# Kernel optimization log

Hardware: AMD Instinct MI355X
Metric: run time of the kernel (lower is better)

Reference implementation:

```python
import jax, jax.numpy as jnp
import numpy as np

H = 1024       # hidden_size
NH = 16        # num heads
HD = H // NH   # head dim
EPS = 1e-12


def setup_inputs() -> dict:
    key = jax.random.key(0)
    ks = jax.random.split(key, 12)
    s = 1.0 / np.sqrt(H)
    return {
        "hidden_states": jax.random.normal(ks[0], (2, 2048, H), jnp.float32),
        "attention_mask": jnp.zeros((2, 1, 1, 2048), jnp.float32),
        "wq": jax.random.uniform(ks[1], (H, H), jnp.float32, -s, s),
        "bq": jnp.zeros((H,), jnp.float32),
        "wk": jax.random.uniform(ks[2], (H, H), jnp.float32, -s, s),
        "bk": jnp.zeros((H,), jnp.float32),
        "wv": jax.random.uniform(ks[3], (H, H), jnp.float32, -s, s),
        "bv": jnp.zeros((H,), jnp.float32),
        "wo": jax.random.uniform(ks[4], (H, H), jnp.float32, -s, s),
        "bo": jnp.zeros((H,), jnp.float32),
        "ln_gamma": jnp.ones((H,), jnp.float32),
        "ln_beta": jnp.zeros((H,), jnp.float32),
    }


def reference(hidden_states, attention_mask, wq, bq, wk, bk, wv, bv, wo, bo, ln_gamma, ln_beta):
    residual = hidden_states
    # pre-LayerNorm
    mu = jnp.mean(hidden_states, axis=-1, keepdims=True)
    var = jnp.var(hidden_states, axis=-1, keepdims=True)
    x = (hidden_states - mu) / jnp.sqrt(var + EPS) * ln_gamma + ln_beta

    B, S, _ = x.shape
    # QKV projections (torch Linear: x @ W.T + b), split heads -> [B, NH, S, HD]
    def proj(w, b):
        return (x @ w.T + b).reshape(B, S, NH, HD).transpose(0, 2, 1, 3)
    q = proj(wq, bq)
    k = proj(wk, bk)
    v = proj(wv, bv)

    scores = jnp.einsum("bhqd,bhkd->bhqk", q, k) / np.sqrt(HD).astype(np.float32)
    scores = scores + attention_mask  # broadcast additive mask
    probs = jax.nn.softmax(scores, axis=-1)
    ctx = jnp.einsum("bhqk,bhkd->bhqd", probs, v)
    ctx = ctx.transpose(0, 2, 1, 3).reshape(B, S, NH * HD)

    out = ctx @ wo.T + bo
    return out + residual
```

## Files before the change

kernel.cpp:

```cpp
#include <hip/hip_runtime.h>
#include <cstdint>

typedef unsigned short u16;
typedef __bf16  bf16x8 __attribute__((ext_vector_type(8)));
typedef unsigned short u16x8 __attribute__((ext_vector_type(8)));
typedef unsigned short u16x4 __attribute__((ext_vector_type(4)));
typedef float   f32x4  __attribute__((ext_vector_type(4)));

#define LOG2E 1.44269504088896340736f

__device__ __forceinline__ u16 f2b(float f) {
  union { __bf16 h; u16 u; } c; c.h = (__bf16)f;
  return c.u;
}

__device__ __forceinline__ int swz(int row) { return (row & 7) ^ ((row >> 3) & 7); }
__device__ __forceinline__ int sidx(int row, int k) {
  return row * 64 + ((((k >> 3) ^ swz(row)) & 7) << 3) + (k & 7);
}
__device__ __forceinline__ bf16x8 ld_frag(const u16* base, int row, int k) {
  return *(const bf16x8*)(base + sidx(row, k));
}

__device__ __forceinline__ void async16(const u16* g, u16* l) {
  __builtin_amdgcn_global_load_lds(
      (__attribute__((address_space(1))) unsigned int*)(uintptr_t)g,
      (__attribute__((address_space(3))) unsigned int*)(uintptr_t)l,
      16, 0, 0);
}

__device__ __forceinline__ void plswap32(unsigned int &a, unsigned int &b) {
  auto r = __builtin_amdgcn_permlane32_swap(a, b, false, false);
  a = r[0]; b = r[1];
}
__device__ __forceinline__ void plswap16(unsigned int &a, unsigned int &b) {
#if __has_builtin(__builtin_amdgcn_permlane16_swap)
  auto r = __builtin_amdgcn_permlane16_swap(a, b, false, false);
  a = r[0]; b = r[1];
#else
  asm volatile("v_permlane16_swap_b32 %0, %1" : "+v"(a), "+v"(b));
#endif
}

__global__ __launch_bounds__(256) void prep_kernel(
    const float* __restrict__ hs, const float* __restrict__ gamma,
    const float* __restrict__ beta, u16* __restrict__ X,
    const float* __restrict__ w0, const float* __restrict__ w1,
    const float* __restrict__ w2, const float* __restrict__ w3,
    u16* __restrict__ Wd) {
  const int tid = threadIdx.x;
  if (blockIdx.x >= 4096) {
    const int idx4 = blockIdx.x - 4096;
    const int mat = idx4 >> 10;
    const float* src = (mat == 0) ? w0 : (mat == 1) ? w1 : (mat == 2) ? w2 : w3;
    const int idx = ((idx4 & 1023) * 256 + tid) * 4;
    f32x4 v = *(const f32x4*)(src + idx);
    u16x4 o;
#pragma unroll
    for (int j = 0; j < 4; ++j) o[j] = f2b(v[j]);
    *(u16x4*)(Wd + (size_t)mat * 1048576 + idx) = o;
    return;
  }
  __shared__ float red[8];
  const int row = blockIdx.x;
  f32x4 v = *(const f32x4*)(hs + (size_t)row * 1024 + tid * 4);
  float s = 0.f, s2 = 0.f;
#pragma unroll
  for (int j = 0; j < 4; ++j) { s += v[j]; s2 += v[j] * v[j]; }
#pragma unroll
  for (int o = 1; o < 64; o <<= 1) { s += __shfl_xor(s, o); s2 += __shfl_xor(s2, o); }
  const int wid = tid >> 6, lane = tid & 63;
  if (lane == 0) { red[wid] = s; red[4 + wid] = s2; }
  __syncthreads();
  s  = red[0] + red[1] + red[2] + red[3];
  s2 = red[4] + red[5] + red[6] + red[7];
  const float mean = s * (1.f / 1024.f);
  const float var  = fmaxf(s2 * (1.f / 1024.f) - mean * mean, 0.f);
  const float rstd = rsqrtf(var + 1e-12f);
  f32x4 g = *(const f32x4*)(gamma + tid * 4);
  f32x4 bb = *(const f32x4*)(beta + tid * 4);
  u16x4 outv;
#pragma unroll
  for (int j = 0; j < 4; ++j) outv[j] = f2b((v[j] - mean) * rstd * g[j] + bb[j]);
  *(u16x4*)(X + (size_t)row * 1024 + tid * 4) = outv;
}

template <int MODE>
__device__ __forceinline__ void gemm_tile_128(
    const u16* __restrict__ A, const u16* __restrict__ Bt,
    const float* __restrict__ bias, const float* __restrict__ res,
    void* __restrict__ Cv, int ldc) {
  __shared__ __align__(16) u16 As[128 * 64];
  __shared__ __align__(16) u16 Bs[128 * 64];
  const int tid = threadIdx.x;
  const int wid = tid >> 6;
  const int lane = tid & 63;
  const int l15 = lane & 15, lq = lane >> 4;
  const int wm = (wid & 1) << 6, wn = (wid >> 1) << 6;
  const int srow = tid >> 3;
  const int sg = tid & 7;

  f32x4 acc[4][4] = {};
  u16x8 ar[4], br[4];

#pragma unroll
  for (int i = 0; i < 4; ++i) {
    int row = (i << 5) + srow;
    ar[i] = *(const u16x8*)(A  + (size_t)row * 1024 + (sg << 3));
    br[i] = *(const u16x8*)(Bt + (size_t)row * 1024 + (sg << 3));
  }

  for (int k0 = 0; k0 < 1024; k0 += 64) {
    if (k0) __syncthreads();
#pragma unroll
    for (int i = 0; i < 4; ++i) {
      int row = (i << 5) + srow;
      *(u16x8*)(As + sidx(row, sg << 3)) = ar[i];
      *(u16x8*)(Bs + sidx(row, sg << 3)) = br[i];
    }
    __syncthreads();
    if (k0 + 64 < 1024) {
#pragma unroll
      for (int i = 0; i < 4; ++i) {
        int row = (i << 5) + srow;
        ar[i] = *(const u16x8*)(A  + (size_t)row * 1024 + k0 + 64 + (sg << 3));
        br[i] = *(const u16x8*)(Bt + (size_t)row * 1024 + k0 + 64 + (sg << 3));
      }
    }
#pragma unroll
    for (int kk = 0; kk < 2; ++kk) {
      bf16x8 af[4], bf[4];
#pragma unroll
      for (int mi = 0; mi < 4; ++mi) af[mi] = ld_frag(As, wm + (mi << 4) + l15, (kk << 5) + (lq << 3));
#pragma unroll
      for (int ni = 0; ni < 4; ++ni) bf[ni] = ld_frag(Bs, wn + (ni << 4) + l15, (kk << 5) + (lq << 3));
#pragma unroll
      for (int mi = 0; mi < 4; ++mi)
#pragma unroll
        for (int ni = 0; ni < 4; ++ni)
          acc[mi][ni] = __builtin_amdgcn_mfma_f32_16x16x32_bf16(af[mi], bf[ni], acc[mi][ni], 0, 0, 0);
    }
  }

#pragma unroll
  for (int ni = 0; ni < 4; ++ni) {
    const int n = wn + (ni << 4) + l15;
    const float bv = bias[n];
#pragma unroll
    for (int mi = 0; mi < 4; ++mi) {
#pragma unroll
      for (int r = 0; r < 4; ++r) {
        const int m = wm + (mi << 4) + (lq << 2) + r;
        float v = acc[mi][ni][r] + bv;
        v += res[(size_t)m * ldc + n];
        ((float*)Cv)[(size_t)m * ldc + n] = v;
      }
    }
  }
}

template <int MODE>
__device__ __forceinline__ void gemm_tile_128_gl(
    const u16* __restrict__ A, const u16* __restrict__ Bt,
    const float* __restrict__ bias,
    void* __restrict__ Cv, int ldc, int m0, int nG) {
  __shared__ __align__(16) u16 Asb[2][128 * 64];
  __shared__ __align__(16) u16 Bsb[2][128 * 64];
  const int tid = threadIdx.x;
  const int wid = tid >> 6;
  const int lane = tid & 63;
  const int l15 = lane & 15, lq = lane >> 4;
  const int wm = (wid & 1) << 6, wn = (wid >> 1) << 6;
  const int lrow = lane >> 3, sg = lane & 7;

  int goff[4], kld[4];
#pragma unroll
  for (int i = 0; i < 4; ++i) {
    const int row = (wid << 5) + (i << 3) + lrow;
    goff[i] = row * 1024 + (((sg ^ swz(row)) & 7) << 3);
    kld[i] = ((wid << 5) + (i << 3)) << 6;
  }

  f32x4 acc[4][4] = {};

#pragma unroll
  for (int i = 0; i < 4; ++i) async16(A  + goff[i], &Asb[0][0] + kld[i]);
#pragma unroll
  for (int i = 0; i < 4; ++i) async16(Bt + goff[i], &Bsb[0][0] + kld[i]);

  for (int k0 = 0; k0 < 1024; k0 += 64) {
    const int buf = (k0 >> 6) & 1;
    __syncthreads();
    if (k0 + 64 < 1024) {
#pragma unroll
      for (int i = 0; i < 4; ++i) async16(A  + goff[i] + k0 + 64, &Asb[buf ^ 1][0] + kld[i]);
#pragma unroll
      for (int i = 0; i < 4; ++i) async16(Bt + goff[i] + k0 + 64, &Bsb[buf ^ 1][0] + kld[i]);
    }
    const u16* As = &Asb[buf][0];
    const u16* Bs = &Bsb[buf][0];
#pragma unroll
    for (int kk = 0; kk < 2; ++kk) {
      bf16x8 af[4], bf[4];
#pragma unroll
      for (int mi = 0; mi < 4; ++mi) af[mi] = ld_frag(As, wm + (mi << 4) + l15, (kk << 5) + (lq << 3));
#pragma unroll
      for (int ni = 0; ni < 4; ++ni) bf[ni] = ld_frag(Bs, wn + (ni << 4) + l15, (kk << 5) + (lq << 3));
#pragma unroll
      for (int mi = 0; mi < 4; ++mi)
#pragma unroll
        for (int ni = 0; ni < 4; ++ni)
          acc[mi][ni] = __builtin_amdgcn_mfma_f32_16x16x32_bf16(af[mi], bf[ni], acc[mi][ni], 0, 0, 0);
    }
  }
  __syncthreads();

  if (MODE == 2) {
    u16* Rg = (wid < 2 ? &Asb[0][0] : &Bsb[0][0]) + ((wid & 1) << 12);
#pragma unroll
    for (int ni = 0; ni < 4; ++ni) {
      const float bv = bias[wn + (ni << 4) + l15];
#pragma unroll
      for (int mi = 0; mi < 4; ++mi) {
        u16x4 pk;
#pragma unroll
        for (int r = 0; r < 4; ++r) pk[r] = f2b(acc[mi][ni][r] + bv);
        *(u16x4*)(Rg + sidx((ni << 4) + l15, (mi << 4) + (lq << 2))) = pk;
      }
    }
    __asm__ volatile("" ::: "memory");
    const int rrow = lane >> 3;
    const int rg8  = (lane & 7) << 3;
    const int mg0 = m0 + wm;
    const int bb = mg0 >> 11, ss0 = mg0 & 2047;
    const int hh = (nG + wn) >> 6;
    u16* vbase = (u16*)Cv + ((size_t)((bb << 4) + hh) * 64) * 2048 + ss0;
#pragma unroll
    for (int p = 0; p < 8; ++p) {
      const int nl = (p << 3) + rrow;
      bf16x8 rowv = ld_frag(Rg, nl, rg8);
      *(bf16x8*)(vbase + (size_t)nl * 2048 + rg8) = rowv;
    }
  } else {
#pragma unroll
    for (int ni = 0; ni < 4; ++ni) {
      const int n = wn + (ni << 4) + l15;
      const float bv = bias[n];
#pragma unroll
      for (int mi = 0; mi < 4; ++mi) {
#pragma unroll
        for (int r = 0; r < 4; ++r) {
          const int m = wm + (mi << 4) + (lq << 2) + r;
          ((u16*)Cv)[(size_t)m * ldc + n] = f2b(acc[mi][ni][r] + bv);
        }
      }
    }
  }
}

__global__ __launch_bounds__(256, 2) void qkv_kernel(
    const u16* __restrict__ X, const u16* __restrict__ W,
    const float* __restrict__ bq, const float* __restrict__ bk, const float* __restrict__ bv,
    u16* __restrict__ QK, u16* __restrict__ VT) {
  const int n0 = blockIdx.x << 7;
  const int m0 = blockIdx.y << 7;
  const int wsel = n0 >> 10;
  const int nloc = n0 & 1023;
  const u16* Bt = W + (size_t)wsel * 1048576 + (size_t)nloc * 1024;
  if (wsel < 2) {
    const float* bias = (wsel == 0 ? bq : bk) + nloc;
    gemm_tile_128_gl<0>(X + (size_t)m0 * 1024, Bt, bias,
                        QK + (size_t)m0 * 2048 + n0, 2048, 0, 0);
  } else {
    gemm_tile_128_gl<2>(X + (size_t)m0 * 1024, Bt, bv + nloc,
                        VT, 0, m0, nloc);
  }
}

__global__ __launch_bounds__(256, 3) void out_kernel(
    const u16* __restrict__ CTX, const u16* __restrict__ wo,
    const float* __restrict__ bo, const float* __restrict__ res, float* __restrict__ OUT) {
  const int n0 = blockIdx.x << 7;
  const int m0 = blockIdx.y << 7;
  gemm_tile_128<1>(CTX + (size_t)m0 * 1024, wo + (size_t)n0 * 1024, bo + n0,
                   res + (size_t)m0 * 1024 + n0, OUT + (size_t)m0 * 1024 + n0, 1024);
}

__global__ __launch_bounds__(256, 2) void attn_kernel(
    const u16* __restrict__ QK, const u16* __restrict__ VT,
    const float* __restrict__ mask, u16* __restrict__ CTX) {
  __shared__ __align__(16) u16 Ksb[2][64 * 64];
  __shared__ __align__(16) u16 Vtsb[2][64 * 64];
  const int tid = threadIdx.x;
  const int wid = tid >> 6;
  const int lane = tid & 63;
  const int l15 = lane & 15, lq = lane >> 4;

  const int lid = blockIdx.x;
  const int sw = ((lid & 7) << 6) | (lid >> 3);
  const int qt = sw & 15;
  const int hz = sw >> 4;
  const int h = hz & 15;
  const int b = hz >> 4;

  const int qbase = (b << 11) + (qt << 7) + (wid << 5);
  const u16* Kbase  = QK + (size_t)(b << 11) * 2048 + 1024 + (h << 6);
  const u16* VTbase = VT + (size_t)(((b << 4) + h) << 6) * 2048;

  bf16x8 qf[2][2];
#pragma unroll
  for (int f = 0; f < 2; ++f)
#pragma unroll
    for (int kc = 0; kc < 2; ++kc)
      qf[f][kc] = *(const bf16x8*)(QK + (size_t)(qbase + (f << 4) + l15) * 2048 + (h << 6) + (kc << 5) + (lq << 3));

  bf16x8 onesf;
#pragma unroll
  for (int j = 0; j < 8; ++j) onesf[j] = (__bf16)1.0f;

  f32x4 cacc[2][4] = {};
  f32x4 lacc[2] = {};

  const int sg = lane & 7;
  const int srow0 = (wid << 4) + (lane >> 3);
  const int srow1 = srow0 + 8;
  const int gk0 = ((sg ^ swz(srow0)) & 7) << 3;
  const int gk1 = ((sg ^ swz(srow1)) & 7) << 3;
  const int ld0 = ((wid << 1) + 0) << 9;
  const int ld1 = ((wid << 1) + 1) << 9;

  async16(Kbase + (size_t)srow0 * 2048 + gk0, &Ksb[0][0] + ld0);
  async16(Kbase + (size_t)srow1 * 2048 + gk1, &Ksb[0][0] + ld1);
  async16(VTbase + (size_t)srow0 * 2048 + gk0, &Vtsb[0][0] + ld0);
  async16(VTbase + (size_t)srow1 * 2048 + gk1, &Vtsb[0][0] + ld1);

  for (int kt = 0; kt < 32; ++kt) {
    const u16* Ks  = &Ksb[kt & 1][0];
    const u16* Vts = &Vtsb[kt & 1][0];
    __syncthreads();
    if (kt + 1 < 32) {
      const int nk = (kt + 1) << 6;
      async16(Kbase + (size_t)(nk + srow0) * 2048 + gk0, &Ksb[(kt + 1) & 1][0] + ld0);
      async16(Kbase + (size_t)(nk + srow1) * 2048 + gk1, &Ksb[(kt + 1) & 1][0] + ld1);
      async16(VTbase + (size_t)srow0 * 2048 + nk + gk0, &Vtsb[(kt + 1) & 1][0] + ld0);
      async16(VTbase + (size_t)srow1 * 2048 + nk + gk1, &Vtsb[(kt + 1) & 1][0] + ld1);
    }

    f32x4 sacc[2][4] = {};
    __builtin_amdgcn_s_setprio(1);
#pragma unroll
    for (int kc = 0; kc < 2; ++kc) {
      bf16x8 kf[4];
#pragma unroll
      for (int ki = 0; ki < 4; ++ki) kf[ki] = ld_frag(Ks, (ki << 4) + l15, (kc << 5) + (lq << 3));
#pragma unroll
      for (int f = 0; f < 2; ++f)
#pragma unroll
        for (int ki = 0; ki < 4; ++ki)
          sacc[f][ki] = __builtin_amdgcn_mfma_f32_16x16x32_bf16(kf[ki], qf[f][kc], sacc[f][ki], 0, 0, 0);
    }
    __builtin_amdgcn_s_setprio(0);

    f32x4 mvl[4];
#pragma unroll
    for (int ki = 0; ki < 4; ++ki) {
      f32x4 mv = *(const f32x4*)(mask + (b << 11) + (kt << 6) + (ki << 4) + (lq << 2));
#pragma unroll
      for (int r = 0; r < 4; ++r) mvl[ki][r] = mv[r] * LOG2E;
    }

    unsigned int w0[2][4], w1[2][4];
#pragma unroll
    for (int f = 0; f < 2; ++f) {
#pragma unroll
      for (int ki = 0; ki < 4; ++ki) {
#pragma unroll
        for (int r = 0; r < 4; ++r)
          sacc[f][ki][r] = __builtin_amdgcn_exp2f(sacc[f][ki][r] * (0.125f * LOG2E) + mvl[ki][r]);
        unsigned int wa, wb;
        asm("v_cvt_pk_bf16_f32 %0, %1, %2" : "=v"(wa) : "v"(sacc[f][ki][0]), "v"(sacc[f][ki][1]));
        asm("v_cvt_pk_bf16_f32 %0, %1, %2" : "=v"(wb) : "v"(sacc[f][ki][2]), "v"(sacc[f][ki][3]));
        w0[f][ki] = wa; w1[f][ki] = wb;
      }
    }

#pragma unroll
    for (int kc = 0; kc < 2; ++kc) {
      bf16x8 pf[2];
#pragma unroll
      for (int f = 0; f < 2; ++f) {
        unsigned int a0 = w0[f][(kc << 1) + 0], a1 = w1[f][(kc << 1) + 0];
        unsigned int b0 = w0[f][(kc << 1) + 1], b1 = w1[f][(kc << 1) + 1];
        plswap32(a0, b0); plswap32(a1, b1);
        plswap16(a0, b0); plswap16(a1, b1);
        union { unsigned int u[4]; bf16x8 v; } pc;
        pc.u[0] = a0; pc.u[1] = a1; pc.u[2] = b0; pc.u[3] = b1;
        pf[f] = pc.v;
      }
      __builtin_amdgcn_s_setprio(1);
#pragma unroll
      for (int dm = 0; dm < 4; ++dm) {
        bf16x8 vf = ld_frag(Vts, (dm << 4) + l15, (kc << 5) + (lq << 3));
#pragma unroll
        for (int f = 0; f < 2; ++f)
          cacc[f][dm] = __builtin_amdgcn_mfma_f32_16x16x32_bf16(vf, pf[f], cacc[f][dm], 0, 0, 0);
      }
#pragma unroll
      for (int f = 0; f < 2; ++f)
        lacc[f] = __builtin_amdgcn_mfma_f32_16x16x32_bf16(onesf, pf[f], lacc[f], 0, 0, 0);
      __builtin_amdgcn_s_setprio(0);
    }
  }

#pragma unroll
  for (int f = 0; f < 2; ++f) {
    const float inv = 1.0f / lacc[f][0];
    u16* Crow = CTX + (size_t)(qbase + (f << 4) + l15) * 1024 + (h << 6);
#pragma unroll
    for (int dm = 0; dm < 4; ++dm) {
      u16x4 o;
#pragma unroll
      for (int r = 0; r < 4; ++r) o[r] = f2b(cacc[f][dm][r] * inv);
      *(u16x4*)(Crow + (dm << 4) + (lq << 2)) = o;
    }
  }
}

extern "C" void kernel_launch(void* const* d_in, const int* in_sizes, int n_in,
                              void* d_out, int out_size, void* d_ws, size_t ws_size,
                              hipStream_t stream) {
  const float* hs   = (const float*)d_in[0];
  const float* mask = (const float*)d_in[1];
  const float* wq   = (const float*)d_in[2];
  const float* bq   = (const float*)d_in[3];
  const float* wk   = (const float*)d_in[4];
  const float* bk   = (const float*)d_in[5];
  const float* wv   = (const float*)d_in[6];
  const float* bv   = (const float*)d_in[7];
  const float* wo   = (const float*)d_in[8];
  const float* bo   = (const float*)d_in[9];
  const float* lg   = (const float*)d_in[10];
  const float* lb   = (const float*)d_in[11];

  u16* X   = (u16*)d_ws;
  u16* QK  = X + (size_t)4096 * 1024;
  u16* CTX = QK + (size_t)4096 * 2048;
  u16* W   = CTX + (size_t)4096 * 1024;
  u16* VT  = W + (size_t)4 * 1048576;
  float* OUT = (float*)d_out;

  prep_kernel<<<8192, 256, 0, stream>>>(hs, lg, lb, X, wq, wk, wv, wo, W);
  qkv_kernel<<<dim3(24, 32), 256, 0, stream>>>(X, W, bq, bk, bv, QK, VT);
  attn_kernel<<<dim3(512), 256, 0, stream>>>(QK, VT, mask, CTX);
  out_kernel<<<dim3(8, 32), 256, 0, stream>>>(CTX, W + (size_t)3 * 1048576, bo, hs, OUT);
}
```

Baseline: 209.8 us.

## Split attention KV loop across two warp halves, narrow out-GEMM tiles, revert QKV pipeline

The attention kernel now runs 512 threads per block. Two groups of four warps each process half of the key range, and the partial context and row sums are merged through shared memory at the end. This doubles waves per query tile to hide latency, at the cost of a combine step and more LDS. The output projection uses 128x64 tiles to launch twice as many blocks. The QKV GEMM switches from the async double-buffered loader back to the register-staged single-buffer tile with a higher occupancy bound, which risks losing load/compute overlap.

After: 224.4 us. 6.9% more time.

```diff
diff --git a/kernel.cpp b/kernel.cpp
--- a/kernel.cpp
+++ b/kernel.cpp
@@ -89,7 +89,7 @@
 __device__ __forceinline__ void gemm_tile_128(
     const u16* __restrict__ A, const u16* __restrict__ Bt,
     const float* __restrict__ bias, const float* __restrict__ res,
-    void* __restrict__ Cv, int ldc) {
+    void* __restrict__ Cv, int ldc, int m0, int nG) {
   __shared__ __align__(16) u16 As[128 * 64];
   __shared__ __align__(16) u16 Bs[128 * 64];
   const int tid = threadIdx.x;
@@ -141,82 +141,10 @@
           acc[mi][ni] = __builtin_amdgcn_mfma_f32_16x16x32_bf16(af[mi], bf[ni], acc[mi][ni], 0, 0, 0);
     }
   }
-
-#pragma unroll
-  for (int ni = 0; ni < 4; ++ni) {
-    const int n = wn + (ni << 4) + l15;
-    const float bv = bias[n];
-#pragma unroll
-    for (int mi = 0; mi < 4; ++mi) {
-#pragma unroll
-      for (int r = 0; r < 4; ++r) {
-        const int m = wm + (mi << 4) + (lq << 2) + r;
-        float v = acc[mi][ni][r] + bv;
-        v += res[(size_t)m * ldc + n];
-        ((float*)Cv)[(size_t)m * ldc + n] = v;
-      }
-    }
-  }
-}
-
-template <int MODE>
-__device__ __forceinline__ void gemm_tile_128_gl(
-    const u16* __restrict__ A, const u16* __restrict__ Bt,
-    const float* __restrict__ bias,
-    void* __restrict__ Cv, int ldc, int m0, int nG) {
-  __shared__ __align__(16) u16 Asb[2][128 * 64];
-  __shared__ __align__(16) u16 Bsb[2][128 * 64];
-  const int tid = threadIdx.x;
-  const int wid = tid >> 6;
-  const int lane = tid & 63;
-  const int l15 = lane & 15, lq = lane >> 4;
-  const int wm = (wid & 1) << 6, wn = (wid >> 1) << 6;
-  const int lrow = lane >> 3, sg = lane & 7;
-
-  int goff[4], kld[4];
-#pragma unroll
-  for (int i = 0; i < 4; ++i) {
-    const int row = (wid << 5) + (i << 3) + lrow;
-    goff[i] = row * 1024 + (((sg ^ swz(row)) & 7) << 3);
-    kld[i] = ((wid << 5) + (i << 3)) << 6;
-  }
-
-  f32x4 acc[4][4] = {};
-
-#pragma unroll
-  for (int i = 0; i < 4; ++i) async16(A  + goff[i], &Asb[0][0] + kld[i]);
-#pragma unroll
-  for (int i = 0; i < 4; ++i) async16(Bt + goff[i], &Bsb[0][0] + kld[i]);
-
-  for (int k0 = 0; k0 < 1024; k0 += 64) {
-    const int buf = (k0 >> 6) & 1;
-    __syncthreads();
-    if (k0 + 64 < 1024) {
-#pragma unroll
-      for (int i = 0; i < 4; ++i) async16(A  + goff[i] + k0 + 64, &Asb[buf ^ 1][0] + kld[i]);
-#pragma unroll
-      for (int i = 0; i < 4; ++i) async16(Bt + goff[i] + k0 + 64, &Bsb[buf ^ 1][0] + kld[i]);
-    }
-    const u16* As = &Asb[buf][0];
-    const u16* Bs = &Bsb[buf][0];
-#pragma unroll
-    for (int kk = 0; kk < 2; ++kk) {
-      bf16x8 af[4], bf[4];
-#pragma unroll
-      for (int mi = 0; mi < 4; ++mi) af[mi] = ld_frag(As, wm + (mi << 4) + l15, (kk << 5) + (lq << 3));
-#pragma unroll
-      for (int ni = 0; ni < 4; ++ni) bf[ni] = ld_frag(Bs, wn + (ni << 4) + l15, (kk << 5) + (lq << 3));
-#pragma unroll
-      for (int mi = 0; mi < 4; ++mi)
-#pragma unroll
-        for (int ni = 0; ni < 4; ++ni)
-          acc[mi][ni] = __builtin_amdgcn_mfma_f32_16x16x32_bf16(af[mi], bf[ni], acc[mi][ni], 0, 0, 0);
-    }
-  }
   __syncthreads();
 
   if (MODE == 2) {
-    u16* Rg = (wid < 2 ? &Asb[0][0] : &Bsb[0][0]) + ((wid & 1) << 12);
+    u16* Rg = (wid < 2 ? As : Bs) + ((wid & 1) << 12);
 #pragma unroll
     for (int ni = 0; ni < 4; ++ni) {
       const float bv = bias[wn + (ni << 4) + l15];
@@ -251,14 +179,91 @@
 #pragma unroll
         for (int r = 0; r < 4; ++r) {
           const int m = wm + (mi << 4) + (lq << 2) + r;
-          ((u16*)Cv)[(size_t)m * ldc + n] = f2b(acc[mi][ni][r] + bv);
+          float v = acc[mi][ni][r] + bv;
+          if (MODE == 1) {
+            v += res[(size_t)m * ldc + n];
+            ((float*)Cv)[(size_t)m * ldc + n] = v;
+          } else {
+            ((u16*)Cv)[(size_t)m * ldc + n] = f2b(v);
+          }
         }
       }
     }
   }
 }
 
-__global__ __launch_bounds__(256, 2) void qkv_kernel(
+__device__ __forceinline__ void gemm_tile_out64(
+    const u16* __restrict__ A, const u16* __restrict__ Bt,
+    const float* __restrict__ bias, const float* __restrict__ res,
+    float* __restrict__ Cv, int ldc) {
+  __shared__ __align__(16) u16 As[128 * 64];
+  __shared__ __align__(16) u16 Bs[64 * 64];
+  const int tid = threadIdx.x;
+  const int wid = tid >> 6;
+  const int lane = tid & 63;
+  const int l15 = lane & 15, lq = lane >> 4;
+  const int wm = (wid & 1) << 6, wn = (wid >> 1) << 5;
+  const int srow = tid >> 3;
+  const int sg = tid & 7;
+
+  f32x4 acc[4][2] = {};
+  u16x8 ar[4], br[2];
+
+#pragma unroll
+  for (int i = 0; i < 4; ++i)
+    ar[i] = *(const u16x8*)(A + (size_t)(((i << 5) + srow)) * 1024 + (sg << 3));
+#pragma unroll
+  for (int i = 0; i < 2; ++i)
+    br[i] = *(const u16x8*)(Bt + (size_t)(((i << 5) + srow)) * 1024 + (sg << 3));
+
+  for (int k0 = 0; k0 < 1024; k0 += 64) {
+    if (k0) __syncthreads();
+#pragma unroll
+    for (int i = 0; i < 4; ++i)
+      *(u16x8*)(As + sidx((i << 5) + srow, sg << 3)) = ar[i];
+#pragma unroll
+    for (int i = 0; i < 2; ++i)
+      *(u16x8*)(Bs + sidx((i << 5) + srow, sg << 3)) = br[i];
+    __syncthreads();
+    if (k0 + 64 < 1024) {
+#pragma unroll
+      for (int i = 0; i < 4; ++i)
+        ar[i] = *(const u16x8*)(A + (size_t)(((i << 5) + srow)) * 1024 + k0 + 64 + (sg << 3));
+#pragma unroll
+      for (int i = 0; i < 2; ++i)
+        br[i] = *(const u16x8*)(Bt + (size_t)(((i << 5) + srow)) * 1024 + k0 + 64 + (sg << 3));
+    }
+#pragma unroll
+    for (int kk = 0; kk < 2; ++kk) {
+      bf16x8 af[4], bf[2];
+#pragma unroll
+      for (int mi = 0; mi < 4; ++mi) af[mi] = ld_frag(As, wm + (mi << 4) + l15, (kk << 5) + (lq << 3));
+#pragma unroll
+      for (int ni = 0; ni < 2; ++ni) bf[ni] = ld_frag(Bs, wn + (ni << 4) + l15, (kk << 5) + (lq << 3));
+#pragma unroll
+      for (int mi = 0; mi < 4; ++mi)
+#pragma unroll
+        for (int ni = 0; ni < 2; ++ni)
+          acc[mi][ni] = __builtin_amdgcn_mfma_f32_16x16x32_bf16(af[mi], bf[ni], acc[mi][ni], 0, 0, 0);
+    }
+  }
+
+#pragma unroll
+  for (int ni = 0; ni < 2; ++ni) {
+    const int n = wn + (ni << 4) + l15;
+    const float bv = bias[n];
+#pragma unroll
+    for (int mi = 0; mi < 4; ++mi) {
+#pragma unroll
+      for (int r = 0; r < 4; ++r) {
+        const int m = wm + (mi << 4) + (lq << 2) + r;
+        Cv[(size_t)m * ldc + n] = acc[mi][ni][r] + bv + res[(size_t)m * ldc + n];
+      }
+    }
+  }
+}
+
+__global__ __launch_bounds__(256, 3) void qkv_kernel(
     const u16* __restrict__ X, const u16* __restrict__ W,
     const float* __restrict__ bq, const float* __restrict__ bk, const float* __restrict__ bv,
     u16* __restrict__ QK, u16* __restrict__ VT) {
@@ -269,30 +274,32 @@
   const u16* Bt = W + (size_t)wsel * 1048576 + (size_t)nloc * 1024;
   if (wsel < 2) {
     const float* bias = (wsel == 0 ? bq : bk) + nloc;
-    gemm_tile_128_gl<0>(X + (size_t)m0 * 1024, Bt, bias,
-                        QK + (size_t)m0 * 2048 + n0, 2048, 0, 0);
+    gemm_tile_128<0>(X + (size_t)m0 * 1024, Bt, bias, nullptr,
+                     QK + (size_t)m0 * 2048 + n0, 2048, 0, 0);
   } else {
-    gemm_tile_128_gl<2>(X + (size_t)m0 * 1024, Bt, bv + nloc,
-                        VT, 0, m0, nloc);
+    gemm_tile_128<2>(X + (size_t)m0 * 1024, Bt, bv + nloc, nullptr,
+                     VT, 0, m0, nloc);
   }
 }
 
 __global__ __launch_bounds__(256, 3) void out_kernel(
     const u16* __restrict__ CTX, const u16* __restrict__ wo,
     const float* __restrict__ bo, const float* __restrict__ res, float* __restrict__ OUT) {
-  const int n0 = blockIdx.x << 7;
+  const int n0 = blockIdx.x << 6;
   const int m0 = blockIdx.y << 7;
-  gemm_tile_128<1>(CTX + (size_t)m0 * 1024, wo + (size_t)n0 * 1024, bo + n0,
-                   res + (size_t)m0 * 1024 + n0, OUT + (size_t)m0 * 1024 + n0, 1024);
-}
-
-__global__ __launch_bounds__(256, 2) void attn_kernel(
+  gemm_tile_out64(CTX + (size_t)m0 * 1024, wo + (size_t)n0 * 1024, bo + n0,
+                  res + (size_t)m0 * 1024 + n0, OUT + (size_t)m0 * 1024 + n0, 1024);
+}
+
+__global__ __launch_bounds__(512, 4) void attn_kernel(
     const u16* __restrict__ QK, const u16* __restrict__ VT,
     const float* __restrict__ mask, u16* __restrict__ CTX) {
-  __shared__ __align__(16) u16 Ksb[2][64 * 64];
-  __shared__ __align__(16) u16 Vtsb[2][64 * 64];
+  __shared__ __align__(16) u16 Ksb[2][2][64 * 64];
+  __shared__ __align__(16) u16 Vtsb[2][2][64 * 64];
   const int tid = threadIdx.x;
   const int wid = tid >> 6;
+  const int half = wid >> 2;
+  const int wid4 = wid & 3;
   const int lane = tid & 63;
   const int l15 = lane & 15, lq = lane >> 4;
 
@@ -303,9 +310,10 @@
   const int h = hz & 15;
   const int b = hz >> 4;
 
-  const int qbase = (b << 11) + (qt << 7) + (wid << 5);
+  const int qbase = (b << 11) + (qt << 7) + (wid4 << 5);
   const u16* Kbase  = QK + (size_t)(b << 11) * 2048 + 1024 + (h << 6);
   const u16* VTbase = VT + (size_t)(((b << 4) + h) << 6) * 2048;
+  const int kt0 = half << 4;
 
   bf16x8 qf[2][2];
 #pragma unroll
@@ -322,29 +330,30 @@
   f32x4 lacc[2] = {};
 
   const int sg = lane & 7;
-  const int srow0 = (wid << 4) + (lane >> 3);
+  const int srow0 = (wid4 << 4) + (lane >> 3);
   const int srow1 = srow0 + 8;
   const int gk0 = ((sg ^ swz(srow0)) & 7) << 3;
   const int gk1 = ((sg ^ swz(srow1)) & 7) << 3;
-  const int ld0 = ((wid << 1) + 0) << 9;
-  const int ld1 = ((wid << 1) + 1) << 9;
-
-  async16(Kbase + (size_t)srow0 * 2048 + gk0, &Ksb[0][0] + ld0);
-  async16(Kbase + (size_t)srow1 * 2048 + gk1, &Ksb[0][0] + ld1);
-  async16(VTbase + (size_t)srow0 * 2048 + gk0, &Vtsb[0][0] + ld0);
-  async16(VTbase + (size_t)srow1 * 2048 + gk1, &Vtsb[0][0] + ld1);
-
-  for (int kt = 0; kt < 32; ++kt) {
-    const u16* Ks  = &Ksb[kt & 1][0];
-    const u16* Vts = &Vtsb[kt & 1][0];
+  const int ld0 = ((wid4 << 1) + 0) << 9;
+  const int ld1 = ((wid4 << 1) + 1) << 9;
+
+  auto STAGE = [&](int lt) {
+    u16* kb = &Ksb[half][lt & 1][0];
+    u16* vb = &Vtsb[half][lt & 1][0];
+    const int nk = (kt0 + lt) << 6;
+    async16(Kbase + (size_t)(nk + srow0) * 2048 + gk0, kb + ld0);
+    async16(Kbase + (size_t)(nk + srow1) * 2048 + gk1, kb + ld1);
+    async16(VTbase + (size_t)srow0 * 2048 + nk + gk0, vb + ld0);
+    async16(VTbase + (size_t)srow1 * 2048 + nk + gk1, vb + ld1);
+  };
+
+  STAGE(0);
+
+  for (int lt = 0; lt < 16; ++lt) {
+    const u16* Ks  = &Ksb[half][lt & 1][0];
+    const u16* Vts = &Vtsb[half][lt & 1][0];
     __syncthreads();
-    if (kt + 1 < 32) {
-      const int nk = (kt + 1) << 6;
-      async16(Kbase + (size_t)(nk + srow0) * 2048 + gk0, &Ksb[(kt + 1) & 1][0] + ld0);
-      async16(Kbase + (size_t)(nk + srow1) * 2048 + gk1, &Ksb[(kt + 1) & 1][0] + ld1);
-      async16(VTbase + (size_t)srow0 * 2048 + nk + gk0, &Vtsb[(kt + 1) & 1][0] + ld0);
-      async16(VTbase + (size_t)srow1 * 2048 + nk + gk1, &Vtsb[(kt + 1) & 1][0] + ld1);
-    }
+    if (lt + 1 < 16) STAGE(lt + 1);
 
     f32x4 sacc[2][4] = {};
     __builtin_amdgcn_s_setprio(1);
@@ -364,7 +373,7 @@
     f32x4 mvl[4];
 #pragma unroll
     for (int ki = 0; ki < 4; ++ki) {
-      f32x4 mv = *(const f32x4*)(mask + (b << 11) + (kt << 6) + (ki << 4) + (lq << 2));
+      f32x4 mv = *(const f32x4*)(mask + (b << 11) + ((kt0 + lt) << 6) + (ki << 4) + (lq << 2));
 #pragma unroll
       for (int r = 0; r < 4; ++r) mvl[ki][r] = mv[r] * LOG2E;
     }
@@ -412,16 +421,38 @@
     }
   }
 
-#pragma unroll
-  for (int f = 0; f < 2; ++f) {
-    const float inv = 1.0f / lacc[f][0];
-    u16* Crow = CTX + (size_t)(qbase + (f << 4) + l15) * 1024 + (h << 6);
-#pragma unroll
-    for (int dm = 0; dm < 4; ++dm) {
-      u16x4 o;
-#pragma unroll
-      for (int r = 0; r < 4; ++r) o[r] = f2b(cacc[f][dm][r] * inv);
-      *(u16x4*)(Crow + (dm << 4) + (lq << 2)) = o;
+  float* CombC = (float*)&Ksb[0][0][0];
+  float* CombL = (float*)&Vtsb[0][0][0];
+  __syncthreads();
+  if (half == 1) {
+    float* dst = CombC + (wid4 << 11) + (lane << 5);
+#pragma unroll
+    for (int j = 0; j < 8; ++j)
+      *(f32x4*)(dst + (((j ^ swz(lane)) & 7) << 2)) = cacc[j >> 2][j & 3];
+    CombL[(wid4 << 7) + (lane << 1) + 0] = lacc[0][0];
+    CombL[(wid4 << 7) + (lane << 1) + 1] = lacc[1][0];
+  }
+  __syncthreads();
+  if (half == 0) {
+    float* src = CombC + (wid4 << 11) + (lane << 5);
+#pragma unroll
+    for (int j = 0; j < 8; ++j) {
+      f32x4 t = *(const f32x4*)(src + (((j ^ swz(lane)) & 7) << 2));
+      cacc[j >> 2][j & 3] += t;
+    }
+    const float l0 = lacc[0][0] + CombL[(wid4 << 7) + (lane << 1) + 0];
+    const float l1 = lacc[1][0] + CombL[(wid4 << 7) + (lane << 1) + 1];
+#pragma unroll
+    for (int f = 0; f < 2; ++f) {
+      const float inv = 1.0f / (f == 0 ? l0 : l1);
+      u16* Crow = CTX + (size_t)(qbase + (f << 4) + l15) * 1024 + (h << 6);
+#pragma unroll
+      for (int dm = 0; dm < 4; ++dm) {
+        u16x4 o;
+#pragma unroll
+        for (int r = 0; r < 4; ++r) o[r] = f2b(cacc[f][dm][r] * inv);
+        *(u16x4*)(Crow + (dm << 4) + (lq << 2)) = o;
+      }
     }
   }
 }
@@ -451,6 +482,6 @@
 
   prep_kernel<<<8192, 256, 0, stream>>>(hs, lg, lb, X, wq, wk, wv, wo, W);
   qkv_kernel<<<dim3(24, 32), 256, 0, stream>>>(X, W, bq, bk, bv, QK, VT);
-  attn_kernel<<<dim3(512), 256, 0, stream>>>(QK, VT, mask, CTX);
-  out_kernel<<<dim3(8, 32), 256, 0, stream>>>(CTX, W + (size_t)3 * 1048576, bo, hs, OUT);
-}
+  attn_kernel<<<dim3(512), 512, 0, stream>>>(QK, VT, mask, CTX);
+  out_kernel<<<dim3(16, 32), 256, 0, stream>>>(CTX, W + (size_t)3 * 1048576, bo, hs, OUT);
+}
```
